# Kernel optimization log

Hardware: AMD Instinct MI355X
Metric: run time of the kernel (lower is better)

Reference implementation:

```python
import jax, jax.numpy as jnp
import numpy as np

ROBOT_W = 1.0
PHASE_W = 1.0
COHER_W = 10.0
SPEED_W = 5.0
MAX_SPEED = 10.0
SMOOTH_VEL_W = 0.05
SMOOTH_ACC_W = 0.01

# illegal phase transitions {(0,2),(1,0),(2,0),(2,1)} as a 3x3 lookup table
_ILLEGAL = np.zeros((3, 3), dtype=bool)
for a, b in [(0, 2), (1, 0), (2, 0), (2, 1)]:
    _ILLEGAL[a, b] = True
ILLEGAL_TABLE = jnp.asarray(_ILLEGAL)


def setup_inputs() -> dict:
    key = jax.random.key(0)
    k1, k2, k3, k4 = jax.random.split(key, 4)
    B, T = 256, 8192
    # scale by 8 so per-frame speeds (norm of diffs of 3-vectors) exceed MAX_SPEED
    pred_robot = jax.random.normal(k1, (B, T, 12), dtype=jnp.float32) * 8.0
    gt_robot = jax.random.normal(k2, (B, T, 12), dtype=jnp.float32) * 8.0
    pred_phase = jax.random.normal(k3, (B, T, 3), dtype=jnp.float32)
    gt_phase = jax.random.randint(k4, (B, T), 0, 3, dtype=jnp.int32)
    return {"pred_robot": pred_robot, "pred_phase": pred_phase,
            "gt_robot": gt_robot, "gt_phase": gt_phase}


def _coherence_loss(phase_logits):
    # vectorized replacement for the O(B*T) Python double loop
    p = jnp.argmax(phase_logits, axis=-1)            # [B, T]
    pt, pt1 = p[:, :-1], p[:, 1:]                    # [B, T-1]
    illegal = ILLEGAL_TABLE[pt, pt1]                 # [B, T-1] bool
    # logit of the (illegal) predicted phase at t+1
    sel = jnp.take_along_axis(phase_logits[:, 1:], pt1[..., None], axis=-1)[..., 0]
    loss_sum = jnp.sum(jnp.where(illegal, sel * sel, 0.0))
    count = jnp.sum(illegal)
    return jnp.where(count > 0, loss_sum / jnp.maximum(count, 1).astype(sel.dtype), 0.0)


def _speed_loss(pred_robot):
    B, T, D = pred_robot.shape
    vel = pred_robot[:, 1:] - pred_robot[:, :-1]     # [B, T-1, 12]
    pts = vel.reshape(B, T - 1, 4, 3)
    speeds = jnp.linalg.norm(pts, axis=-1)           # [B, T-1, 4]
    pen = jax.nn.relu(speeds - MAX_SPEED)
    return SPEED_W * jnp.mean(pen * pen)


def reference(pred_robot, pred_phase, gt_robot, gt_phase):
    # MSE over robot trajectory
    robot_loss = jnp.mean((pred_robot - gt_robot) ** 2)
    # cross-entropy over 3 phase classes
    logp = jax.nn.log_softmax(pred_phase, axis=-1)   # [B, T, 3]
    nll = -jnp.take_along_axis(logp, gt_phase[..., None].astype(jnp.int32), axis=-1)[..., 0]
    phase_loss = jnp.mean(nll)
    coherence = _coherence_loss(pred_phase)
    speed_loss = _speed_loss(pred_robot)
    vel = pred_robot[:, 1:] - pred_robot[:, :-1]
    vel_loss = jnp.mean(vel * vel)
    acc = pred_robot[:, 2:] - 2.0 * pred_robot[:, 1:-1] + pred_robot[:, :-2]
    acc_loss = jnp.mean(acc * acc)
    total = (ROBOT_W * robot_loss + PHASE_W * phase_loss + COHER_W * coherence
             + speed_loss + SMOOTH_VEL_W * vel_loss + SMOOTH_ACC_W * acc_loss)
    return total
```

## Files before the change

### kernel.cpp

```cpp
#include <hip/hip_runtime.h>
#include <math.h>

#define B_DIM 256
#define T_DIM 8192
#define BLOCK 256
#define CHUNKS_PER_B (T_DIM / BLOCK)
#define NSLOT 256


__global__ __launch_bounds__(BLOCK) void combined_loss_main(
    const float4* __restrict__ pred4,
    const float*  __restrict__ pred_phase,
    const float4* __restrict__ gt4,
    const int*    __restrict__ gt_phase,
    double* __restrict__ ws)
{
    __shared__ float4 sp[774];
    __shared__ float  s_ph[776];
    __shared__ float  s_red[4][8];

    const int tid   = threadIdx.x;
    const int b     = blockIdx.x >> 5;
    const int chunk = blockIdx.x & 31;
    const int t0    = chunk << 8;
    const int t     = t0 + tid;

    const size_t row0  = (size_t)b * T_DIM + t0;
    const size_t base4 = row0 * 3;
    const float4* ph4  = (const float4*)pred_phase + ((row0 * 3) >> 2);
    const bool halo = (t0 + BLOCK) < T_DIM;

    float4 p0 = pred4[base4 + tid];
    float4 p1 = pred4[base4 + tid + 256];
    float4 p2 = pred4[base4 + tid + 512];
    float4 g0 = gt4[base4 + tid];
    float4 g1 = gt4[base4 + tid + 256];
    float4 g2 = gt4[base4 + tid + 512];
    float4 ph = make_float4(0.f, 0.f, 0.f, 0.f);
    if (tid < 192) ph = ph4[tid];
    const int gidx = gt_phase[row0 + tid];
    if (halo && tid >= 248 && tid < 254)
        sp[768 + (tid - 248)] = pred4[base4 + 768 + (tid - 248)];
    if (halo && tid >= 192 && tid < 198)
        s_ph[768 + (tid - 192)] = pred_phase[row0 * 3 + 768 + (tid - 192)];

    float sse = 0.0f;
    {
        float d;
        d = p0.x - g0.x; sse += d*d;  d = p0.y - g0.y; sse += d*d;
        d = p0.z - g0.z; sse += d*d;  d = p0.w - g0.w; sse += d*d;
        d = p1.x - g1.x; sse += d*d;  d = p1.y - g1.y; sse += d*d;
        d = p1.z - g1.z; sse += d*d;  d = p1.w - g1.w; sse += d*d;
        d = p2.x - g2.x; sse += d*d;  d = p2.y - g2.y; sse += d*d;
        d = p2.z - g2.z; sse += d*d;  d = p2.w - g2.w; sse += d*d;
    }

    sp[tid]       = p0;
    sp[tid + 256] = p1;
    sp[tid + 512] = p2;
    if (tid < 192) *((float4*)&s_ph[4 * tid]) = ph;
    __syncthreads();

    const float l0 = s_ph[3*tid], l1 = s_ph[3*tid + 1], l2 = s_ph[3*tid + 2];
    float m = fmaxf(l0, fmaxf(l1, l2));
    float lse = m + logf(expf(l0 - m) + expf(l1 - m) + expf(l2 - m));
    float sel = (gidx == 0) ? l0 : ((gidx == 1) ? l1 : l2);
    float nll = lse - sel;

    int p = 0; float pm = l0;
    if (l1 > pm) { pm = l1; p = 1; }
    if (l2 > pm) { pm = l2; p = 2; }

    float csum = 0.0f, ccnt = 0.0f, pen2 = 0.0f, velsq = 0.0f, accsq = 0.0f;

    float4 a0 = sp[tid*3], a1 = sp[tid*3 + 1], a2 = sp[tid*3 + 2];
    float rA[12] = { a0.x,a0.y,a0.z,a0.w, a1.x,a1.y,a1.z,a1.w, a2.x,a2.y,a2.z,a2.w };

    if (t < T_DIM - 1) {
        float4 b0 = sp[tid*3 + 3], b1 = sp[tid*3 + 4], b2 = sp[tid*3 + 5];
        float rB[12] = { b0.x,b0.y,b0.z,b0.w, b1.x,b1.y,b1.z,b1.w, b2.x,b2.y,b2.z,b2.w };

        float vel[12];
        #pragma unroll
        for (int k = 0; k < 12; ++k) { vel[k] = rB[k] - rA[k]; velsq += vel[k]*vel[k]; }

        #pragma unroll
        for (int j = 0; j < 4; ++j) {
            float sx = vel[3*j], sy = vel[3*j+1], sz = vel[3*j+2];
            float sp2 = sqrtf(sx*sx + sy*sy + sz*sz);
            float d = sp2 - 10.0f;
            if (d > 0.0f) pen2 += d*d;
        }

        float n0 = s_ph[3*tid + 3], n1 = s_ph[3*tid + 4], n2 = s_ph[3*tid + 5];
        int p1i = 0; float m1 = n0;
        if (n1 > m1) { m1 = n1; p1i = 1; }
        if (n2 > m1) { m1 = n2; p1i = 2; }
        int mask = (p == 0) ? 4 : ((p == 1) ? 1 : 3);
        if ((mask >> p1i) & 1) { csum += m1*m1; ccnt += 1.0f; }

        if (t < T_DIM - 2) {
            float4 c0 = sp[tid*3 + 6], c1 = sp[tid*3 + 7], c2 = sp[tid*3 + 8];
            float rC[12] = { c0.x,c0.y,c0.z,c0.w, c1.x,c1.y,c1.z,c1.w, c2.x,c2.y,c2.z,c2.w };
            #pragma unroll
            for (int k = 0; k < 12; ++k) {
                float a = rC[k] - 2.0f*rB[k] + rA[k];
                accsq += a*a;
            }
        }
    }

    float vals[7] = { sse, nll, csum, ccnt, pen2, velsq, accsq };
    #pragma unroll
    for (int off = 32; off > 0; off >>= 1) {
        #pragma unroll
        for (int q = 0; q < 7; ++q)
            vals[q] += __shfl_down(vals[q], off, 64);
    }
    const int wave = tid >> 6, lane = tid & 63;
    if (lane == 0) {
        #pragma unroll
        for (int q = 0; q < 7; ++q) s_red[wave][q] = vals[q];
    }
    __syncthreads();
    if (tid < 7) {
        double acc = (double)s_red[0][tid] + (double)s_red[1][tid]
                   + (double)s_red[2][tid] + (double)s_red[3][tid];
        atomicAdd(&ws[(size_t)(blockIdx.x & (NSLOT - 1)) * 8 + tid], acc);
    }
}

__global__ __launch_bounds__(256) void combined_loss_final(
    const double* __restrict__ ws, float* __restrict__ out)
{
    __shared__ double sred[4][7];
    const int tid = threadIdx.x;
    double v[7];
    #pragma unroll
    for (int q = 0; q < 7; ++q) v[q] = ws[(size_t)tid * 8 + q];
    #pragma unroll
    for (int off = 32; off > 0; off >>= 1) {
        #pragma unroll
        for (int q = 0; q < 7; ++q)
            v[q] += __shfl_down(v[q], off, 64);
    }
    const int wave = tid >> 6, lane = tid & 63;
    if (lane == 0) {
        #pragma unroll
        for (int q = 0; q < 7; ++q) sred[wave][q] = v[q];
    }
    __syncthreads();
    if (tid == 0) {
        double s[7];
        #pragma unroll
        for (int q = 0; q < 7; ++q)
            s[q] = sred[0][q] + sred[1][q] + sred[2][q] + sred[3][q];
        const double robot = s[0] / (double)((size_t)B_DIM * T_DIM * 12);
        const double phase = s[1] / (double)((size_t)B_DIM * T_DIM);
        const double coher = (s[3] > 0.0) ? (s[2] / fmax(s[3], 1.0)) : 0.0;
        const double speed = 5.0  * (s[4] / (double)((size_t)B_DIM * (T_DIM - 1) * 4));
        const double vel   = 0.05 * (s[5] / (double)((size_t)B_DIM * (T_DIM - 1) * 12));
        const double acc   = 0.01 * (s[6] / (double)((size_t)B_DIM * (T_DIM - 2) * 12));
        out[0] = (float)(robot + phase + 10.0 * coher + speed + vel + acc);
    }
}

extern "C" void kernel_launch(void* const* d_in, const int* in_sizes, int n_in,
                              void* d_out, int out_size, void* d_ws, size_t ws_size,
                              hipStream_t stream)
{
    const float4* pred4      = (const float4*)d_in[0];
    const float*  pred_phase = (const float*)d_in[1];
    const float4* gt4        = (const float4*)d_in[2];
    const int*    gt_phase   = (const int*)d_in[3];
    double* ws  = (double*)d_ws;
    float*  out = (float*)d_out;

    hipMemsetAsync(d_ws, 0, (size_t)NSLOT * 8 * sizeof(double), stream);

    const dim3 grid(B_DIM * CHUNKS_PER_B);
    combined_loss_main<<<grid, BLOCK, 0, stream>>>(pred4, pred_phase, gt4, gt_phase, ws);
    combined_loss_final<<<1, 256, 0, stream>>>(ws, out);
}
```

Measured before the change: 240.1 us.

## Replace shared-memory staging with direct per-thread neighbor loads from global memory

Removes the LDS staging of robot and phase data and the block barrier; each thread now loads its own row plus the next two rows directly from global memory, relying on L1/L2 caching for the overlap. This drops the shared-memory traffic and synchronisation but triples the global load requests for pred_robot and issues strided non-coalesced per-thread float4 loads (48-byte stride), which may reduce coalescing efficiency.

```diff
diff --git a/kernel.cpp b/kernel.cpp
--- a/kernel.cpp
+++ b/kernel.cpp
@@ -4,8 +4,8 @@
 #define B_DIM 256
 #define T_DIM 8192
 #define BLOCK 256
-#define CHUNKS_PER_B (T_DIM / BLOCK)
 #define NSLOT 256
+#define GRID_BLOCKS 8192
 
 
 __global__ __launch_bounds__(BLOCK) void combined_loss_main(
@@ -15,97 +15,83 @@
     const int*    __restrict__ gt_phase,
     double* __restrict__ ws)
 {
-    __shared__ float4 sp[774];
-    __shared__ float  s_ph[776];
-    __shared__ float  s_red[4][8];
+    __shared__ float s_red[4][8];
 
-    const int tid   = threadIdx.x;
-    const int b     = blockIdx.x >> 5;
-    const int chunk = blockIdx.x & 31;
-    const int t0    = chunk << 8;
-    const int t     = t0 + tid;
+    const int tid = threadIdx.x;
+    const int r   = (int)blockIdx.x * BLOCK + tid;
+    const int t   = r & (T_DIM - 1);
+    const bool v1 = (t < T_DIM - 1);
+    const bool v2 = (t < T_DIM - 2);
 
-    const size_t row0  = (size_t)b * T_DIM + t0;
-    const size_t base4 = row0 * 3;
-    const float4* ph4  = (const float4*)pred_phase + ((row0 * 3) >> 2);
-    const bool halo = (t0 + BLOCK) < T_DIM;
+    const float4* pr = pred4 + (size_t)r * 3;
+    const float4* gr = gt4   + (size_t)r * 3;
+    const float*  pp = pred_phase + (size_t)r * 3;
 
-    float4 p0 = pred4[base4 + tid];
-    float4 p1 = pred4[base4 + tid + 256];
-    float4 p2 = pred4[base4 + tid + 512];
-    float4 g0 = gt4[base4 + tid];
-    float4 g1 = gt4[base4 + tid + 256];
-    float4 g2 = gt4[base4 + tid + 512];
-    float4 ph = make_float4(0.f, 0.f, 0.f, 0.f);
-    if (tid < 192) ph = ph4[tid];
-    const int gidx = gt_phase[row0 + tid];
-    if (halo && tid >= 248 && tid < 254)
-        sp[768 + (tid - 248)] = pred4[base4 + 768 + (tid - 248)];
-    if (halo && tid >= 192 && tid < 198)
-        s_ph[768 + (tid - 192)] = pred_phase[row0 * 3 + 768 + (tid - 192)];
+    const int o1 = v1 ? 3 : 0;
+    const int o2 = v2 ? 6 : 0;
+
+    float4 a0 = pr[0],      a1 = pr[1],      a2 = pr[2];
+    float4 b0 = pr[o1],     b1 = pr[o1 + 1], b2 = pr[o1 + 2];
+    float4 c0 = pr[o2],     c1 = pr[o2 + 1], c2 = pr[o2 + 2];
+    float4 q0 = gr[0],      q1 = gr[1],      q2 = gr[2];
+
+    const float l0 = pp[0],  l1 = pp[1],  l2 = pp[2];
+    const float n0 = pp[o1], n1 = pp[o1 + 1], n2 = pp[o1 + 2];
+    const int gidx = gt_phase[r];
 
     float sse = 0.0f;
     {
         float d;
-        d = p0.x - g0.x; sse += d*d;  d = p0.y - g0.y; sse += d*d;
-        d = p0.z - g0.z; sse += d*d;  d = p0.w - g0.w; sse += d*d;
-        d = p1.x - g1.x; sse += d*d;  d = p1.y - g1.y; sse += d*d;
-        d = p1.z - g1.z; sse += d*d;  d = p1.w - g1.w; sse += d*d;
-        d = p2.x - g2.x; sse += d*d;  d = p2.y - g2.y; sse += d*d;
-        d = p2.z - g2.z; sse += d*d;  d = p2.w - g2.w; sse += d*d;
+        d = a0.x - q0.x; sse += d*d;  d = a0.y - q0.y; sse += d*d;
+        d = a0.z - q0.z; sse += d*d;  d = a0.w - q0.w; sse += d*d;
+        d = a1.x - q1.x; sse += d*d;  d = a1.y - q1.y; sse += d*d;
+        d = a1.z - q1.z; sse += d*d;  d = a1.w - q1.w; sse += d*d;
+        d = a2.x - q2.x; sse += d*d;  d = a2.y - q2.y; sse += d*d;
+        d = a2.z - q2.z; sse += d*d;  d = a2.w - q2.w; sse += d*d;
     }
 
-    sp[tid]       = p0;
-    sp[tid + 256] = p1;
-    sp[tid + 512] = p2;
-    if (tid < 192) *((float4*)&s_ph[4 * tid]) = ph;
-    __syncthreads();
-
-    const float l0 = s_ph[3*tid], l1 = s_ph[3*tid + 1], l2 = s_ph[3*tid + 2];
     float m = fmaxf(l0, fmaxf(l1, l2));
     float lse = m + logf(expf(l0 - m) + expf(l1 - m) + expf(l2 - m));
     float sel = (gidx == 0) ? l0 : ((gidx == 1) ? l1 : l2);
     float nll = lse - sel;
 
-    int p = 0; float pm = l0;
-    if (l1 > pm) { pm = l1; p = 1; }
-    if (l2 > pm) { pm = l2; p = 2; }
+    float csum = 0.0f, ccnt = 0.0f;
+    if (v1) {
+        int p = 0; float pm = l0;
+        if (l1 > pm) { pm = l1; p = 1; }
+        if (l2 > pm) { pm = l2; p = 2; }
+        int p1 = 0; float m1 = n0;
+        if (n1 > m1) { m1 = n1; p1 = 1; }
+        if (n2 > m1) { m1 = n2; p1 = 2; }
+        int mask = (p == 0) ? 4 : ((p == 1) ? 1 : 3);
+        if ((mask >> p1) & 1) { csum = m1 * m1; ccnt = 1.0f; }
+    }
 
-    float csum = 0.0f, ccnt = 0.0f, pen2 = 0.0f, velsq = 0.0f, accsq = 0.0f;
+    float pen2 = 0.0f, velsq = 0.0f, accsq = 0.0f;
+    {
+        float rA[12] = { a0.x,a0.y,a0.z,a0.w, a1.x,a1.y,a1.z,a1.w, a2.x,a2.y,a2.z,a2.w };
+        float rB[12] = { b0.x,b0.y,b0.z,b0.w, b1.x,b1.y,b1.z,b1.w, b2.x,b2.y,b2.z,b2.w };
+        float rC[12] = { c0.x,c0.y,c0.z,c0.w, c1.x,c1.y,c1.z,c1.w, c2.x,c2.y,c2.z,c2.w };
 
-    float4 a0 = sp[tid*3], a1 = sp[tid*3 + 1], a2 = sp[tid*3 + 2];
-    float rA[12] = { a0.x,a0.y,a0.z,a0.w, a1.x,a1.y,a1.z,a1.w, a2.x,a2.y,a2.z,a2.w };
+        if (v1) {
+            float vel[12];
+            #pragma unroll
+            for (int k = 0; k < 12; ++k) { vel[k] = rB[k] - rA[k]; velsq += vel[k]*vel[k]; }
 
-    if (t < T_DIM - 1) {
-        float4 b0 = sp[tid*3 + 3], b1 = sp[tid*3 + 4], b2 = sp[tid*3 + 5];
-        float rB[12] = { b0.x,b0.y,b0.z,b0.w, b1.x,b1.y,b1.z,b1.w, b2.x,b2.y,b2.z,b2.w };
+            #pragma unroll
+            for (int j = 0; j < 4; ++j) {
+                float sx = vel[3*j], sy = vel[3*j+1], sz = vel[3*j+2];
+                float sp = sqrtf(sx*sx + sy*sy + sz*sz);
+                float d = sp - 10.0f;
+                if (d > 0.0f) pen2 += d*d;
+            }
 
-        float vel[12];
-        #pragma unroll
-        for (int k = 0; k < 12; ++k) { vel[k] = rB[k] - rA[k]; velsq += vel[k]*vel[k]; }
-
-        #pragma unroll
-        for (int j = 0; j < 4; ++j) {
-            float sx = vel[3*j], sy = vel[3*j+1], sz = vel[3*j+2];
-            float sp2 = sqrtf(sx*sx + sy*sy + sz*sz);
-            float d = sp2 - 10.0f;
-            if (d > 0.0f) pen2 += d*d;
-        }
-
-        float n0 = s_ph[3*tid + 3], n1 = s_ph[3*tid + 4], n2 = s_ph[3*tid + 5];
-        int p1i = 0; float m1 = n0;
-        if (n1 > m1) { m1 = n1; p1i = 1; }
-        if (n2 > m1) { m1 = n2; p1i = 2; }
-        int mask = (p == 0) ? 4 : ((p == 1) ? 1 : 3);
-        if ((mask >> p1i) & 1) { csum += m1*m1; ccnt += 1.0f; }
-
-        if (t < T_DIM - 2) {
-            float4 c0 = sp[tid*3 + 6], c1 = sp[tid*3 + 7], c2 = sp[tid*3 + 8];
-            float rC[12] = { c0.x,c0.y,c0.z,c0.w, c1.x,c1.y,c1.z,c1.w, c2.x,c2.y,c2.z,c2.w };
-            #pragma unroll
-            for (int k = 0; k < 12; ++k) {
-                float a = rC[k] - 2.0f*rB[k] + rA[k];
-                accsq += a*a;
+            if (v2) {
+                #pragma unroll
+                for (int k = 0; k < 12; ++k) {
+                    float a = rC[k] - 2.0f*rB[k] + rA[k];
+                    accsq += a*a;
+                }
             }
         }
     }
@@ -178,7 +164,6 @@
 
     hipMemsetAsync(d_ws, 0, (size_t)NSLOT * 8 * sizeof(double), stream);
 
-    const dim3 grid(B_DIM * CHUNKS_PER_B);
-    combined_loss_main<<<grid, BLOCK, 0, stream>>>(pred4, pred_phase, gt4, gt_phase, ws);
+    combined_loss_main<<<dim3(GRID_BLOCKS), BLOCK, 0, stream>>>(pred4, pred_phase, gt4, gt_phase, ws);
     combined_loss_final<<<1, 256, 0, stream>>>(ws, out);
 }
```

New measurement: 237.7 us. No clear change (-1.0%).
